# Performance work log

Measured on AMD Instinct MI355X. Metric: run time of the kernel, lower is better.

The kernel has to match this reference:

```python
import jax, jax.numpy as jnp
import numpy as np

N_SUPPORT = 12800
N_QUERY = 32768
SEQ_LEN = 100
INPUT_DIM = 32
EMBED_DIM = 64
N_CLASSES = 128
EPS = 1e-8


def setup_inputs() -> dict:
    key = jax.random.key(0)
    k1, k2, k3 = jax.random.split(key, 3)
    support = jax.random.normal(k1, (N_SUPPORT, SEQ_LEN, INPUT_DIM), dtype=jnp.float32)
    query = jax.random.normal(k2, (N_QUERY, SEQ_LEN, INPUT_DIM), dtype=jnp.float32)
    # equal shots per class; unique() first-occurrence order == 0..C-1
    support_labels = jnp.arange(N_SUPPORT, dtype=jnp.int64 if jax.config.jax_enable_x64 else jnp.int32) % N_CLASSES
    W = jax.random.normal(k3, (INPUT_DIM, EMBED_DIM), dtype=jnp.float32) * (1.0 / np.sqrt(INPUT_DIM))
    b = jnp.zeros((EMBED_DIM,), dtype=jnp.float32)
    return {"support": support, "support_labels": support_labels, "query": query, "W": W, "b": b}


def _encode(x, W, b):
    # minimal encoder: mean-pool over seq, then linear projection
    return jnp.mean(x, axis=1) @ W + b  # (n, embed_dim)


def reference(support, support_labels, query, W, b):
    se = _encode(support, W, b)   # (n_support, D)
    qe = _encode(query, W, b)     # (n_query, D)
    # per-class mean (segment mean), single fused pass instead of per-class boolean_mask loop
    sums = jax.ops.segment_sum(se, support_labels, num_segments=N_CLASSES)          # (C, D)
    counts = jax.ops.segment_sum(jnp.ones((se.shape[0],), se.dtype), support_labels, num_segments=N_CLASSES)
    prototypes = sums / counts[:, None]                                             # (C, D)
    # pairwise euclidean distance, faithful to expand-subtract-sum formulation
    diff = qe[:, None, :] - prototypes[None, :, :]                                  # (n_query, C, D)
    distances = jnp.sqrt(jnp.sum(diff * diff, axis=2) + EPS)                        # (n_query, C)
    logits = -jnp.square(distances)
    return logits, prototypes
```

## Files before the change

### kernel.cpp

```cpp
#include <hip/hip_runtime.h>

#define SEQ_LEN   100
#define IN_DIM    32
#define EMB       64
#define NCLS      128
#define N_SUPPORT 12800
#define N_QUERY   32768
#define EPS_F     1e-8f


__global__ __launch_bounds__(256) void zero_ws_k(float* __restrict__ ws, int n) {
    int i = blockIdx.x * 256 + threadIdx.x;
    if (i < n) ws[i] = 0.0f;
}


__device__ inline float4 wave_pool(const float* __restrict__ src, int item, int lane) {
    const int d4 = lane & 7;
    const int ph = lane >> 3;
    const float4* base = reinterpret_cast<const float4*>(src)
                       + (size_t)item * (SEQ_LEN * IN_DIM / 4) + d4;
    float4 acc = make_float4(0.f, 0.f, 0.f, 0.f);
    for (int r = ph; r < SEQ_LEN; r += 8) {
        float4 v = base[r * (IN_DIM / 4)];
        acc.x += v.x; acc.y += v.y; acc.z += v.z; acc.w += v.w;
    }
    #pragma unroll
    for (int m = 8; m <= 32; m <<= 1) {
        acc.x += __shfl_xor(acc.x, m);
        acc.y += __shfl_xor(acc.y, m);
        acc.z += __shfl_xor(acc.z, m);
        acc.w += __shfl_xor(acc.w, m);
    }
    return acc;
}

__global__ __launch_bounds__(256) void support_accum_k(
    const float* __restrict__ support, const int* __restrict__ labels,
    float* __restrict__ classSum, float* __restrict__ classCount)
{
    __shared__ float pooled[4][IN_DIM];
    const int t = threadIdx.x;
    const int wave = t >> 6, lane = t & 63;
    const int item0 = blockIdx.x * 4;

    float4 acc = wave_pool(support, item0 + wave, lane);
    if (lane < 8) {
        const float s = 1.0f / (float)SEQ_LEN;
        pooled[wave][lane * 4 + 0] = acc.x * s;
        pooled[wave][lane * 4 + 1] = acc.y * s;
        pooled[wave][lane * 4 + 2] = acc.z * s;
        pooled[wave][lane * 4 + 3] = acc.w * s;
    }
    __syncthreads();
    if (t < 4 * IN_DIM) {
        const int li = t >> 5, k = t & 31;
        const int lab = labels[item0 + li];
        atomicAdd(&classSum[lab * IN_DIM + k], pooled[li][k]);
        if (k == 0) atomicAdd(&classCount[lab], 1.0f);
    }
}

__global__ __launch_bounds__(256) void proto_finalize_k(
    const float* __restrict__ classSum, const float* __restrict__ classCount,
    const float* __restrict__ W, const float* __restrict__ b,
    float* __restrict__ protoOut)
{
    const int idx = blockIdx.x * 256 + threadIdx.x;
    const int c = idx >> 6;
    const int d = idx & 63;
    const float cnt = classCount[c];
    const float inv = (cnt > 0.f) ? (1.0f / cnt) : 0.f;
    float acc = b[d];
    #pragma unroll
    for (int k = 0; k < IN_DIM; ++k)
        acc += classSum[c * IN_DIM + k] * inv * W[k * EMB + d];
    protoOut[idx] = acc;
}

__global__ __launch_bounds__(256) void query_encode_k(
    const float* __restrict__ query, const float* __restrict__ W,
    const float* __restrict__ b, float* __restrict__ qe)
{
    __shared__ float Wl[IN_DIM * EMB];
    __shared__ float pooled[4][IN_DIM];
    const int t = threadIdx.x;
    const int wave = t >> 6, lane = t & 63;
    const int q0 = blockIdx.x * 4;

    #pragma unroll
    for (int j = 0; j < 8; ++j) Wl[t + j * 256] = W[t + j * 256];

    float4 acc = wave_pool(query, q0 + wave, lane);
    if (lane < 8) {
        const float s = 1.0f / (float)SEQ_LEN;
        pooled[wave][lane * 4 + 0] = acc.x * s;
        pooled[wave][lane * 4 + 1] = acc.y * s;
        pooled[wave][lane * 4 + 2] = acc.z * s;
        pooled[wave][lane * 4 + 3] = acc.w * s;
    }
    __syncthreads();

    const int q = t >> 6, d = t & 63;
    float a2 = b[d];
    #pragma unroll
    for (int k = 0; k < IN_DIM; ++k)
        a2 += pooled[q][k] * Wl[k * EMB + d];
    qe[(size_t)(q0 + q) * EMB + d] = a2;
}

__global__ __launch_bounds__(256) void distances_k(
    const float* __restrict__ qe, const float* __restrict__ proto,
    float* __restrict__ logits)
{
    __shared__ float pl[NCLS * (EMB + 1)];
    __shared__ float ql[16 * EMB];
    const int t = threadIdx.x;
    const int q0 = blockIdx.x * 16;

    #pragma unroll
    for (int j = 0; j < 32; ++j) {
        const int i = t + j * 256;
        pl[(i >> 6) * (EMB + 1) + (i & 63)] = proto[i];
    }
    #pragma unroll
    for (int j = 0; j < 4; ++j) {
        const int i = t + j * 256;
        ql[i] = qe[(size_t)q0 * EMB + i];
    }
    __syncthreads();

    float* outB = logits + (size_t)q0 * NCLS;
    #pragma unroll
    for (int j = 0; j < 8; ++j) {
        const int idx = t + j * 256;
        const int q = idx >> 7;
        const int c = idx & 127;
        const float* qv = ql + q * EMB;
        const float* pv = pl + c * (EMB + 1);
        float s2 = 0.f;
        #pragma unroll
        for (int d = 0; d < EMB; ++d) {
            float df = qv[d] - pv[d];
            s2 += df * df;
        }
        outB[idx] = -(s2 + EPS_F);
    }
}

__global__ __launch_bounds__(256) void query_logits_fused_k(
    const float* __restrict__ query, const float* __restrict__ W,
    const float* __restrict__ b, const float* __restrict__ proto,
    float* __restrict__ logits)
{
    __shared__ float Wl[IN_DIM * EMB];
    __shared__ float pl[NCLS * (EMB + 1)];
    __shared__ float pooled[4][IN_DIM];
    __shared__ float qel[4 * EMB];
    const int t = threadIdx.x;
    const int wave = t >> 6, lane = t & 63;
    const int q0 = blockIdx.x * 4;

    #pragma unroll
    for (int j = 0; j < 8; ++j) Wl[t + j * 256] = W[t + j * 256];
    #pragma unroll
    for (int j = 0; j < 32; ++j) {
        const int i = t + j * 256;
        pl[(i >> 6) * (EMB + 1) + (i & 63)] = proto[i];
    }

    float4 acc = wave_pool(query, q0 + wave, lane);
    if (lane < 8) {
        const float s = 1.0f / (float)SEQ_LEN;
        pooled[wave][lane * 4 + 0] = acc.x * s;
        pooled[wave][lane * 4 + 1] = acc.y * s;
        pooled[wave][lane * 4 + 2] = acc.z * s;
        pooled[wave][lane * 4 + 3] = acc.w * s;
    }
    __syncthreads();
    {
        const int q = t >> 6, d = t & 63;
        float a2 = b[d];
        #pragma unroll
        for (int k = 0; k < IN_DIM; ++k)
            a2 += pooled[q][k] * Wl[k * EMB + d];
        qel[t] = a2;
    }
    __syncthreads();
    float* outB = logits + (size_t)q0 * NCLS;
    #pragma unroll
    for (int j = 0; j < 2; ++j) {
        const int idx = t + j * 256;
        const int q = idx >> 7;
        const int c = idx & 127;
        const float* qv = qel + q * EMB;
        const float* pv = pl + c * (EMB + 1);
        float s2 = 0.f;
        #pragma unroll
        for (int d = 0; d < EMB; ++d) {
            float df = qv[d] - pv[d];
            s2 += df * df;
        }
        outB[idx] = -(s2 + EPS_F);
    }
}

extern "C" void kernel_launch(void* const* d_in, const int* in_sizes, int n_in,
                              void* d_out, int out_size, void* d_ws, size_t ws_size,
                              hipStream_t stream) {
    const float* support = (const float*)d_in[0];
    const int*   labels  = (const int*)d_in[1];
    const float* query   = (const float*)d_in[2];
    const float* W       = (const float*)d_in[3];
    const float* b       = (const float*)d_in[4];

    float* out      = (float*)d_out;
    float* logits   = out;
    float* protoOut = out + (size_t)N_QUERY * NCLS;

    float* classSum   = (float*)d_ws;
    float* classCount = classSum + NCLS * IN_DIM;
    float* qeWs       = classCount + NCLS;
    const int nZero = NCLS * IN_DIM + NCLS;
    const size_t wsNeeded = (size_t)(nZero + N_QUERY * EMB) * sizeof(float);

    zero_ws_k<<<(nZero + 255) / 256, 256, 0, stream>>>(classSum, nZero);
    support_accum_k<<<N_SUPPORT / 4, 256, 0, stream>>>(support, labels, classSum, classCount);
    proto_finalize_k<<<(NCLS * EMB) / 256, 256, 0, stream>>>(classSum, classCount, W, b, protoOut);

    if (ws_size >= wsNeeded) {
        query_encode_k<<<N_QUERY / 4, 256, 0, stream>>>(query, W, b, qeWs);
        distances_k<<<N_QUERY / 16, 256, 0, stream>>>(qeWs, protoOut, logits);
    } else {
        query_logits_fused_k<<<N_QUERY / 4, 256, 0, stream>>>(query, W, b, protoOut, logits);
    }
}
```

Measured before the change: 245.3 us.

## Fuse support and query encoding into one persistent grid-stride kernel

```diff
diff --git a/kernel.cpp b/kernel.cpp
--- a/kernel.cpp
+++ b/kernel.cpp
@@ -6,6 +6,7 @@
 #define NCLS      128
 #define N_SUPPORT 12800
 #define N_QUERY   32768
+#define N_ITEMS   (N_SUPPORT + N_QUERY)
 #define EPS_F     1e-8f
 
 
@@ -14,8 +15,139 @@
     if (i < n) ws[i] = 0.0f;
 }
 
-
-__device__ inline float4 wave_pool(const float* __restrict__ src, int item, int lane) {
+__global__ __launch_bounds__(256) void encode_all_k(
+    const float* __restrict__ support, const int* __restrict__ labels,
+    const float* __restrict__ query,   const float* __restrict__ W,
+    const float* __restrict__ b,
+    float* __restrict__ classSum, float* __restrict__ classCount,
+    float* __restrict__ qe)
+{
+    __shared__ float Wl[IN_DIM * EMB];
+    const int t = threadIdx.x;
+    #pragma unroll
+    for (int j = 0; j < 8; ++j) Wl[t + j * 256] = W[t + j * 256];
+
+    const int lane = t & 63;
+    const int wave = t >> 6;
+    const int d4 = lane & 7;
+    const int ph = lane >> 3;
+    const float bd = b[lane];
+    __syncthreads();
+
+    const int nWaves = gridDim.x * 4;
+    const float s = 1.0f / (float)SEQ_LEN;
+
+    for (int item = blockIdx.x * 4 + wave; item < N_ITEMS; item += nWaves) {
+        const bool isSup = item < N_SUPPORT;
+        const float* src = isSup
+            ? support + (size_t)item * (SEQ_LEN * IN_DIM)
+            : query   + (size_t)(item - N_SUPPORT) * (SEQ_LEN * IN_DIM);
+        const float4* base = reinterpret_cast<const float4*>(src) + d4;
+
+        float4 acc = make_float4(0.f, 0.f, 0.f, 0.f);
+        #pragma unroll
+        for (int i = 0; i < 12; ++i) {
+            float4 v = base[(ph + 8 * i) * (IN_DIM / 4)];
+            acc.x += v.x; acc.y += v.y; acc.z += v.z; acc.w += v.w;
+        }
+        if (ph < 4) {
+            float4 v = base[(ph + 96) * (IN_DIM / 4)];
+            acc.x += v.x; acc.y += v.y; acc.z += v.z; acc.w += v.w;
+        }
+        #pragma unroll
+        for (int m = 8; m <= 32; m <<= 1) {
+            acc.x += __shfl_xor(acc.x, m);
+            acc.y += __shfl_xor(acc.y, m);
+            acc.z += __shfl_xor(acc.z, m);
+            acc.w += __shfl_xor(acc.w, m);
+        }
+        acc.x *= s; acc.y *= s; acc.z *= s; acc.w *= s;
+
+        if (isSup) {
+            const int lab = labels[item];
+            if (lane < 8) {
+                float* dst = classSum + lab * IN_DIM + lane * 4;
+                atomicAdd(dst + 0, acc.x);
+                atomicAdd(dst + 1, acc.y);
+                atomicAdd(dst + 2, acc.z);
+                atomicAdd(dst + 3, acc.w);
+            }
+            if (lane == 0) atomicAdd(&classCount[lab], 1.0f);
+        } else {
+            float a2 = bd;
+            #pragma unroll
+            for (int k4 = 0; k4 < 8; ++k4) {
+                const float px = __shfl(acc.x, k4);
+                const float py = __shfl(acc.y, k4);
+                const float pz = __shfl(acc.z, k4);
+                const float pw = __shfl(acc.w, k4);
+                a2 += px * Wl[(k4 * 4 + 0) * EMB + lane];
+                a2 += py * Wl[(k4 * 4 + 1) * EMB + lane];
+                a2 += pz * Wl[(k4 * 4 + 2) * EMB + lane];
+                a2 += pw * Wl[(k4 * 4 + 3) * EMB + lane];
+            }
+            qe[(size_t)(item - N_SUPPORT) * EMB + lane] = a2;
+        }
+    }
+}
+
+__global__ __launch_bounds__(256) void proto_finalize_k(
+    const float* __restrict__ classSum, const float* __restrict__ classCount,
+    const float* __restrict__ W, const float* __restrict__ b,
+    float* __restrict__ protoOut)
+{
+    const int idx = blockIdx.x * 256 + threadIdx.x;
+    const int c = idx >> 6;
+    const int d = idx & 63;
+    const float cnt = classCount[c];
+    const float inv = (cnt > 0.f) ? (1.0f / cnt) : 0.f;
+    float acc = b[d];
+    #pragma unroll
+    for (int k = 0; k < IN_DIM; ++k)
+        acc += classSum[c * IN_DIM + k] * inv * W[k * EMB + d];
+    protoOut[idx] = acc;
+}
+
+__global__ __launch_bounds__(256) void distances_k(
+    const float* __restrict__ qe, const float* __restrict__ proto,
+    float* __restrict__ logits)
+{
+    __shared__ float pl[NCLS * (EMB + 1)];
+    __shared__ float ql[16 * EMB];
+    const int t = threadIdx.x;
+    const int q0 = blockIdx.x * 16;
+
+    #pragma unroll
+    for (int j = 0; j < 32; ++j) {
+        const int i = t + j * 256;
+        pl[(i >> 6) * (EMB + 1) + (i & 63)] = proto[i];
+    }
+    #pragma unroll
+    for (int j = 0; j < 4; ++j) {
+        const int i = t + j * 256;
+        ql[i] = qe[(size_t)q0 * EMB + i];
+    }
+    __syncthreads();
+
+    float* outB = logits + (size_t)q0 * NCLS;
+    #pragma unroll
+    for (int j = 0; j < 8; ++j) {
+        const int idx = t + j * 256;
+        const int q = idx >> 7;
+        const int c = idx & 127;
+        const float* qv = ql + q * EMB;
+        const float* pv = pl + c * (EMB + 1);
+        float s2 = 0.f;
+        #pragma unroll
+        for (int d = 0; d < EMB; ++d) {
+            float df = qv[d] - pv[d];
+            s2 += df * df;
+        }
+        outB[idx] = -(s2 + EPS_F);
+    }
+}
+
+__device__ inline float4 wave_pool_fb(const float* __restrict__ src, int item, int lane) {
     const int d4 = lane & 7;
     const int ph = lane >> 3;
     const float4* base = reinterpret_cast<const float4*>(src)
@@ -35,117 +167,24 @@
     return acc;
 }
 
-__global__ __launch_bounds__(256) void support_accum_k(
+__global__ __launch_bounds__(256) void support_accum_fb_k(
     const float* __restrict__ support, const int* __restrict__ labels,
     float* __restrict__ classSum, float* __restrict__ classCount)
 {
-    __shared__ float pooled[4][IN_DIM];
     const int t = threadIdx.x;
     const int wave = t >> 6, lane = t & 63;
-    const int item0 = blockIdx.x * 4;
-
-    float4 acc = wave_pool(support, item0 + wave, lane);
+    const int item = blockIdx.x * 4 + wave;
+    float4 acc = wave_pool_fb(support, item, lane);
+    const float s = 1.0f / (float)SEQ_LEN;
+    const int lab = labels[item];
     if (lane < 8) {
-        const float s = 1.0f / (float)SEQ_LEN;
-        pooled[wave][lane * 4 + 0] = acc.x * s;
-        pooled[wave][lane * 4 + 1] = acc.y * s;
-        pooled[wave][lane * 4 + 2] = acc.z * s;
-        pooled[wave][lane * 4 + 3] = acc.w * s;
-    }
-    __syncthreads();
-    if (t < 4 * IN_DIM) {
-        const int li = t >> 5, k = t & 31;
-        const int lab = labels[item0 + li];
-        atomicAdd(&classSum[lab * IN_DIM + k], pooled[li][k]);
-        if (k == 0) atomicAdd(&classCount[lab], 1.0f);
-    }
-}
-
-__global__ __launch_bounds__(256) void proto_finalize_k(
-    const float* __restrict__ classSum, const float* __restrict__ classCount,
-    const float* __restrict__ W, const float* __restrict__ b,
-    float* __restrict__ protoOut)
-{
-    const int idx = blockIdx.x * 256 + threadIdx.x;
-    const int c = idx >> 6;
-    const int d = idx & 63;
-    const float cnt = classCount[c];
-    const float inv = (cnt > 0.f) ? (1.0f / cnt) : 0.f;
-    float acc = b[d];
-    #pragma unroll
-    for (int k = 0; k < IN_DIM; ++k)
-        acc += classSum[c * IN_DIM + k] * inv * W[k * EMB + d];
-    protoOut[idx] = acc;
-}
-
-__global__ __launch_bounds__(256) void query_encode_k(
-    const float* __restrict__ query, const float* __restrict__ W,
-    const float* __restrict__ b, float* __restrict__ qe)
-{
-    __shared__ float Wl[IN_DIM * EMB];
-    __shared__ float pooled[4][IN_DIM];
-    const int t = threadIdx.x;
-    const int wave = t >> 6, lane = t & 63;
-    const int q0 = blockIdx.x * 4;
-
-    #pragma unroll
-    for (int j = 0; j < 8; ++j) Wl[t + j * 256] = W[t + j * 256];
-
-    float4 acc = wave_pool(query, q0 + wave, lane);
-    if (lane < 8) {
-        const float s = 1.0f / (float)SEQ_LEN;
-        pooled[wave][lane * 4 + 0] = acc.x * s;
-        pooled[wave][lane * 4 + 1] = acc.y * s;
-        pooled[wave][lane * 4 + 2] = acc.z * s;
-        pooled[wave][lane * 4 + 3] = acc.w * s;
-    }
-    __syncthreads();
-
-    const int q = t >> 6, d = t & 63;
-    float a2 = b[d];
-    #pragma unroll
-    for (int k = 0; k < IN_DIM; ++k)
-        a2 += pooled[q][k] * Wl[k * EMB + d];
-    qe[(size_t)(q0 + q) * EMB + d] = a2;
-}
-
-__global__ __launch_bounds__(256) void distances_k(
-    const float* __restrict__ qe, const float* __restrict__ proto,
-    float* __restrict__ logits)
-{
-    __shared__ float pl[NCLS * (EMB + 1)];
-    __shared__ float ql[16 * EMB];
-    const int t = threadIdx.x;
-    const int q0 = blockIdx.x * 16;
-
-    #pragma unroll
-    for (int j = 0; j < 32; ++j) {
-        const int i = t + j * 256;
-        pl[(i >> 6) * (EMB + 1) + (i & 63)] = proto[i];
-    }
-    #pragma unroll
-    for (int j = 0; j < 4; ++j) {
-        const int i = t + j * 256;
-        ql[i] = qe[(size_t)q0 * EMB + i];
-    }
-    __syncthreads();
-
-    float* outB = logits + (size_t)q0 * NCLS;
-    #pragma unroll
-    for (int j = 0; j < 8; ++j) {
-        const int idx = t + j * 256;
-        const int q = idx >> 7;
-        const int c = idx & 127;
-        const float* qv = ql + q * EMB;
-        const float* pv = pl + c * (EMB + 1);
-        float s2 = 0.f;
-        #pragma unroll
-        for (int d = 0; d < EMB; ++d) {
-            float df = qv[d] - pv[d];
-            s2 += df * df;
-        }
-        outB[idx] = -(s2 + EPS_F);
-    }
+        float* dst = classSum + lab * IN_DIM + lane * 4;
+        atomicAdd(dst + 0, acc.x * s);
+        atomicAdd(dst + 1, acc.y * s);
+        atomicAdd(dst + 2, acc.z * s);
+        atomicAdd(dst + 3, acc.w * s);
+    }
+    if (lane == 0) atomicAdd(&classCount[lab], 1.0f);
 }
 
 __global__ __launch_bounds__(256) void query_logits_fused_k(
@@ -155,7 +194,6 @@
 {
     __shared__ float Wl[IN_DIM * EMB];
     __shared__ float pl[NCLS * (EMB + 1)];
-    __shared__ float pooled[4][IN_DIM];
     __shared__ float qel[4 * EMB];
     const int t = threadIdx.x;
     const int wave = t >> 6, lane = t & 63;
@@ -168,24 +206,22 @@
         const int i = t + j * 256;
         pl[(i >> 6) * (EMB + 1) + (i & 63)] = proto[i];
     }
-
-    float4 acc = wave_pool(query, q0 + wave, lane);
-    if (lane < 8) {
-        const float s = 1.0f / (float)SEQ_LEN;
-        pooled[wave][lane * 4 + 0] = acc.x * s;
-        pooled[wave][lane * 4 + 1] = acc.y * s;
-        pooled[wave][lane * 4 + 2] = acc.z * s;
-        pooled[wave][lane * 4 + 3] = acc.w * s;
-    }
-    __syncthreads();
-    {
-        const int q = t >> 6, d = t & 63;
-        float a2 = b[d];
-        #pragma unroll
-        for (int k = 0; k < IN_DIM; ++k)
-            a2 += pooled[q][k] * Wl[k * EMB + d];
-        qel[t] = a2;
-    }
+    float4 acc = wave_pool_fb(query, q0 + wave, lane);
+    const float s = 1.0f / (float)SEQ_LEN;
+    acc.x *= s; acc.y *= s; acc.z *= s; acc.w *= s;
+    float a2 = b[lane];
+    #pragma unroll
+    for (int k4 = 0; k4 < 8; ++k4) {
+        const float px = __shfl(acc.x, k4);
+        const float py = __shfl(acc.y, k4);
+        const float pz = __shfl(acc.z, k4);
+        const float pw = __shfl(acc.w, k4);
+        a2 += px * Wl[(k4 * 4 + 0) * EMB + lane];
+        a2 += py * Wl[(k4 * 4 + 1) * EMB + lane];
+        a2 += pz * Wl[(k4 * 4 + 2) * EMB + lane];
+        a2 += pw * Wl[(k4 * 4 + 3) * EMB + lane];
+    }
+    qel[t] = a2;
     __syncthreads();
     float* outB = logits + (size_t)q0 * NCLS;
     #pragma unroll
@@ -225,13 +261,15 @@
     const size_t wsNeeded = (size_t)(nZero + N_QUERY * EMB) * sizeof(float);
 
     zero_ws_k<<<(nZero + 255) / 256, 256, 0, stream>>>(classSum, nZero);
-    support_accum_k<<<N_SUPPORT / 4, 256, 0, stream>>>(support, labels, classSum, classCount);
-    proto_finalize_k<<<(NCLS * EMB) / 256, 256, 0, stream>>>(classSum, classCount, W, b, protoOut);
 
     if (ws_size >= wsNeeded) {
-        query_encode_k<<<N_QUERY / 4, 256, 0, stream>>>(query, W, b, qeWs);
+        encode_all_k<<<2048, 256, 0, stream>>>(support, labels, query, W, b,
+                                               classSum, classCount, qeWs);
+        proto_finalize_k<<<(NCLS * EMB) / 256, 256, 0, stream>>>(classSum, classCount, W, b, protoOut);
         distances_k<<<N_QUERY / 16, 256, 0, stream>>>(qeWs, protoOut, logits);
     } else {
+        support_accum_fb_k<<<N_SUPPORT / 4, 256, 0, stream>>>(support, labels, classSum, classCount);
+        proto_finalize_k<<<(NCLS * EMB) / 256, 256, 0, stream>>>(classSum, classCount, W, b, protoOut);
         query_logits_fused_k<<<N_QUERY / 4, 256, 0, stream>>>(query, W, b, protoOut, logits);
     }
 }
```

New measurement: 243.6 us. About the same (-0.7%).
